# Optimization experiments

Hardware: AMD Instinct MI355X
Metric: run time of the kernel (lower is better)

## Reference

```python
import jax, jax.numpy as jnp
import numpy as np

B, N, S, CIN, COUT, GDIM = 4, 128, 8, 8, 8, 7  # batch, points, coset samples, channels, g_embed+2*q_embed


def setup_inputs() -> dict:
    key = jax.random.key(0)
    ks = jax.random.split(key, 8)
    pairwise_g = jax.random.normal(ks[0], (B, N, N, S, S, GDIM), jnp.float32)
    coset_functions = jax.random.normal(ks[1], (B, N, S, CIN), jnp.float32)
    mask = jax.random.bernoulli(ks[2], 0.9, (B, N, S))  # bool key mask (B,N,S)
    # per-channel SumKernel params: k_y = Linear(2->1), k_g = Linear(GDIM->1), stacked over CIN channels
    w_y = jax.random.normal(ks[3], (CIN, 2), jnp.float32) * 0.1
    b_y = jax.random.normal(ks[4], (CIN,), jnp.float32) * 0.1
    w_g = jax.random.normal(ks[5], (CIN, GDIM), jnp.float32) * 0.1
    b_g = jax.random.normal(ks[6], (CIN,), jnp.float32) * 0.1
    w_lin = jax.random.normal(ks[7], (COUT, CIN), jnp.float32) * (1.0 / np.sqrt(CIN))
    return {"pairwise_g": pairwise_g, "coset_functions": coset_functions, "mask": mask,
            "w_y": w_y, "b_y": b_y, "w_g": w_g, "b_g": b_g, "w_lin": w_lin}


def reference(pairwise_g, coset_functions, mask, w_y, b_y, w_g, b_g, w_lin):
    # Vectorized over the original per-channel Python loop: channel axis c.
    y = coset_functions  # (B, N, S, C)
    # k_g(pairwise_g) per channel + both biases: (B,i,j,s1,s2,C)
    logits = jnp.einsum('bijstg,cg->bijstc', pairwise_g, w_g) + (b_g + b_y)
    # k_y([y_1, y_2]): y_1 indexed by key (j, s2) -> weight w_y[:,0]; y_2 by query (i, s1) -> w_y[:,1]
    key_term = y * w_y[:, 0]   # (B, N, S, C)
    qry_term = y * w_y[:, 1]   # (B, N, S, C)
    logits = logits + key_term[:, None, :, None, :, :] + qry_term[:, :, None, :, None, :]
    # plain exp (original does NOT subtract a max), zero out masked keys (j, s2)
    att = jnp.where(mask[:, None, :, None, :, None], jnp.exp(logits), 0.0)
    att = att / att.sum(axis=(2, 4), keepdims=True)  # normalize over key dims
    # weighted sum of key values over (j, s2), residual add
    out = y + jnp.einsum('bijstc,bjtc->bisc', att, y)
    out = out * mask[..., None].astype(out.dtype)
    # output linear c_in -> c_out, no bias (torch Linear: x @ W.T)
    return out @ w_lin.T
```

## Files before the change

### kernel.cpp

```cpp
#include <hip/hip_runtime.h>


namespace {

constexpr int kN = 128, kS = 8, kC = 8, kO = 8, kG = 7;
constexpr int JSTRIDE = 68;

__global__ __launch_bounds__(512, 4)
void emha_kernel(const float* __restrict__ pg,
                 const float* __restrict__ y,
                 const int*   __restrict__ mask,
                 const float* __restrict__ w_y,
                 const float* __restrict__ w_g,
                 const float* __restrict__ w_lin,
                 float*       __restrict__ out)
{
    __shared__ float lds_kw[kN * JSTRIDE];
    __shared__ float lds_kv[kN * JSTRIDE];
    __shared__ float red[8][8][16];
    __shared__ float obuf[8][8];

    const int t  = threadIdx.x;
    const int bi = blockIdx.x;
    const int b  = bi >> 7;
    const int i  = bi & 127;

    float wg[kC][kG];
#pragma unroll
    for (int c = 0; c < kC; ++c)
#pragma unroll
        for (int g = 0; g < kG; ++g)
            wg[c][g] = w_g[c * kG + g];

    const float* yb = y    + b * (kN * kS * kC);
    const int*   mb = mask + b * (kN * kS);
    const float  wy0 = w_y[2 * (t & 7)];
#pragma unroll
    for (int k = 0; k < 16; ++k) {
        const int idx = t + k * 512;
        const float yv = yb[idx];
        const int   m  = mb[idx >> 3];
        const float kw = m ? __expf(yv * wy0) : 0.0f;
        const int off = (idx >> 6) * JSTRIDE + (idx & 63);
        lds_kw[off] = kw;
        lds_kv[off] = kw * yv;
    }
    __syncthreads();

    const int jbase = t >> 3;
    const float* pb = pg + (size_t)bi * (kN * kS * kS * kG) + (size_t)t * 56;
    float num[kC], den[kC];
#pragma unroll
    for (int c = 0; c < kC; ++c) { num[c] = 0.0f; den[c] = 0.0f; }

#pragma unroll 1
    for (int k = 0; k < 2; ++k) {
        const int j = k * 64 + jbase;
        const float* ppair = pb + k * 28672;
#pragma unroll
        for (int h = 0; h < 2; ++h) {
            float4 buf[7];
            const float4* src = reinterpret_cast<const float4*>(ppair + h * 28);
#pragma unroll
            for (int q = 0; q < 7; ++q) buf[q] = src[q];
            const float* p = reinterpret_cast<const float*>(buf);

#pragma unroll
            for (int s2i = 0; s2i < 4; ++s2i) {
                const int lo = j * JSTRIDE + (h * 4 + s2i) * 8;
                const float4 kva = *reinterpret_cast<const float4*>(&lds_kv[lo]);
                const float4 kvb = *reinterpret_cast<const float4*>(&lds_kv[lo + 4]);
                const float4 kwa = *reinterpret_cast<const float4*>(&lds_kw[lo]);
                const float4 kwb = *reinterpret_cast<const float4*>(&lds_kw[lo + 4]);
                const float kv[8] = {kva.x, kva.y, kva.z, kva.w, kvb.x, kvb.y, kvb.z, kvb.w};
                const float kw[8] = {kwa.x, kwa.y, kwa.z, kwa.w, kwb.x, kwb.y, kwb.z, kwb.w};
#pragma unroll
                for (int c = 0; c < kC; ++c) {
                    float d =      p[s2i * kG + 0] * wg[c][0];
                    d = fmaf(p[s2i * kG + 1], wg[c][1], d);
                    d = fmaf(p[s2i * kG + 2], wg[c][2], d);
                    d = fmaf(p[s2i * kG + 3], wg[c][3], d);
                    d = fmaf(p[s2i * kG + 4], wg[c][4], d);
                    d = fmaf(p[s2i * kG + 5], wg[c][5], d);
                    d = fmaf(p[s2i * kG + 6], wg[c][6], d);
                    const float e = __expf(d);
                    num[c] = fmaf(e, kv[c], num[c]);
                    den[c] = fmaf(e, kw[c], den[c]);
                }
            }
        }
    }

#pragma unroll
    for (int c = 0; c < kC; ++c) {
        num[c] += __shfl_xor(num[c], 8);
        num[c] += __shfl_xor(num[c], 16);
        num[c] += __shfl_xor(num[c], 32);
        den[c] += __shfl_xor(den[c], 8);
        den[c] += __shfl_xor(den[c], 16);
        den[c] += __shfl_xor(den[c], 32);
    }
    const int wave = t >> 6;
    const int lane = t & 63;
    if (lane < 8) {
#pragma unroll
        for (int c = 0; c < kC; ++c) {
            red[wave][lane][c]     = num[c];
            red[wave][lane][c + 8] = den[c];
        }
    }
    __syncthreads();

    if (t < 64) {
        const int s1q = t >> 3, c = t & 7;
        float ns = 0.0f, ds = 0.0f;
#pragma unroll
        for (int w = 0; w < 8; ++w) { ns += red[w][s1q][c]; ds += red[w][s1q][c + 8]; }
        const float yv = yb[(i * kS + s1q) * kC + c];
        const int   m  = mb[i * kS + s1q];
        obuf[s1q][c] = m ? (yv + ns / ds) : 0.0f;
    }
    __syncthreads();

    if (t < 64) {
        const int s1q = t >> 3, o = t & 7;
        float acc = 0.0f;
#pragma unroll
        for (int c = 0; c < kC; ++c)
            acc = fmaf(obuf[s1q][c], w_lin[o * kC + c], acc);
        out[(size_t)bi * (kS * kO) + t] = acc;
    }
}

}

extern "C" void kernel_launch(void* const* d_in, const int* in_sizes, int n_in,
                              void* d_out, int out_size, void* d_ws, size_t ws_size,
                              hipStream_t stream)
{
    const float* pg    = (const float*)d_in[0];
    const float* y     = (const float*)d_in[1];
    const int*   mask  = (const int*)  d_in[2];
    const float* w_y   = (const float*)d_in[3];
    const float* w_g   = (const float*)d_in[5];
    const float* w_lin = (const float*)d_in[7];
    float* out = (float*)d_out;

    emha_kernel<<<4 * kN, 512, 0, stream>>>(pg, y, mask, w_y, w_g, w_lin, out);
}
```

Before: 29.22 us.

## Stream pairwise_g via async global-to-LDS loads with per-wave double-stage pipeline

Each wave now owns a contiguous 16-j slab of pairwise_g. It stages that slab into LDS with global_load_lds in four chunks and prefetches the next chunk while computing the current one. The per-block key weight/value table is replaced by per-wave tiles computed just in time, which removes the initial block-wide barrier. Weights are pinned to SGPRs with readfirstlane. The cost is manual waitcnt and sched_barrier management, a fully serialized wait each iteration, and a different reduction lane mapping.

```diff
diff --git a/kernel.cpp b/kernel.cpp
--- a/kernel.cpp
+++ b/kernel.cpp
@@ -3,8 +3,15 @@
 
 namespace {
 
-constexpr int kN = 128, kS = 8, kC = 8, kO = 8, kG = 7;
-constexpr int JSTRIDE = 68;
+constexpr int kC = 8, kO = 8, kG = 7;
+
+typedef const __attribute__((address_space(1))) unsigned int* gp_t;
+typedef __attribute__((address_space(3))) unsigned int* lp_t;
+
+__device__ __forceinline__ float sgpr_pin(float x) {
+    return __int_as_float(__builtin_amdgcn_readfirstlane(__float_as_int(x)));
+}
+
 
 __global__ __launch_bounds__(512, 4)
 void emha_kernel(const float* __restrict__ pg,
@@ -15,110 +22,152 @@
                  const float* __restrict__ w_lin,
                  float*       __restrict__ out)
 {
-    __shared__ float lds_kw[kN * JSTRIDE];
-    __shared__ float lds_kv[kN * JSTRIDE];
-    __shared__ float red[8][8][16];
-    __shared__ float obuf[8][8];
+    __shared__ __align__(16) float arena[19776];
 
     const int t  = threadIdx.x;
+    const int w  = t >> 6;
+    const int l  = t & 63;
     const int bi = blockIdx.x;
     const int b  = bi >> 7;
     const int i  = bi & 127;
 
+    float* pay  = arena + w * 1792;
+    float* kwT  = arena + 14336 + w * 272;
+    float* kvT  = arena + 16512 + w * 272;
+    float* red  = arena + 18688;
+    float* obuf = arena + 19712;
+
+    const float* slab = pg + (size_t)bi * 57344;
+    const float* yb   = y    + b * 8192;
+    const int*   mb   = mask + b * 1024;
+
+    float wy0[kC];
+#pragma unroll
+    for (int c = 0; c < kC; ++c) wy0[c] = sgpr_pin(w_y[2 * c]);
     float wg[kC][kG];
 #pragma unroll
     for (int c = 0; c < kC; ++c)
 #pragma unroll
-        for (int g = 0; g < kG; ++g)
-            wg[c][g] = w_g[c * kG + g];
+        for (int g = 0; g < kG; ++g) wg[c][g] = sgpr_pin(w_g[c * kG + g]);
 
-    const float* yb = y    + b * (kN * kS * kC);
-    const int*   mb = mask + b * (kN * kS);
-    const float  wy0 = w_y[2 * (t & 7)];
+    const int w16 = l & 15;
+    const int jy  = l >> 4;
+    const int s2y = w16 >> 1;
+    const int cb  = (w16 & 1) * 4;
+    const int jl  = l >> 4;
+    const int h   = l & 1;
+
+    auto stage = [&](int g) {
+        const float* src = slab + (size_t)(w * 128 + g * 32) * 56 + l * 4;
 #pragma unroll
-    for (int k = 0; k < 16; ++k) {
-        const int idx = t + k * 512;
-        const float yv = yb[idx];
-        const int   m  = mb[idx >> 3];
-        const float kw = m ? __expf(yv * wy0) : 0.0f;
-        const int off = (idx >> 6) * JSTRIDE + (idx & 63);
-        lds_kw[off] = kw;
-        lds_kv[off] = kw * yv;
-    }
-    __syncthreads();
+        for (int q = 0; q < 7; ++q)
+            __builtin_amdgcn_global_load_lds((gp_t)(src + q * 256),
+                                             (lp_t)(pay + q * 256), 16, 0, 0);
+    };
 
-    const int jbase = t >> 3;
-    const float* pb = pg + (size_t)bi * (kN * kS * kS * kG) + (size_t)t * 56;
+    float4 yv; int mv;
+    auto loady = [&](int g) {
+        const int jg = 16 * w + 4 * g + jy;
+        yv = *reinterpret_cast<const float4*>(yb + jg * 64 + w16 * 4);
+        mv = mb[jg * 8 + s2y];
+    };
+
+    stage(0);
+    loady(0);
+
     float num[kC], den[kC];
 #pragma unroll
     for (int c = 0; c < kC; ++c) { num[c] = 0.0f; den[c] = 0.0f; }
 
 #pragma unroll 1
-    for (int k = 0; k < 2; ++k) {
-        const int j = k * 64 + jbase;
-        const float* ppair = pb + k * 28672;
+    for (int g = 0; g < 4; ++g) {
+        asm volatile("s_waitcnt vmcnt(0)" ::: "memory");
+        __builtin_amdgcn_sched_barrier(0);
+
+        {
+            const float yv4[4] = {yv.x, yv.y, yv.z, yv.w};
+            float kwq[4], kvq[4];
 #pragma unroll
-        for (int h = 0; h < 2; ++h) {
-            float4 buf[7];
-            const float4* src = reinterpret_cast<const float4*>(ppair + h * 28);
+            for (int k = 0; k < 4; ++k) {
+                const float e = __expf(yv4[k] * wy0[cb + k]);
+                kwq[k] = mv ? e : 0.0f;
+                kvq[k] = kwq[k] * yv4[k];
+            }
+            const int toff = jy * 68 + w16 * 4;
+            *reinterpret_cast<float4*>(kwT + toff) =
+                make_float4(kwq[0], kwq[1], kwq[2], kwq[3]);
+            *reinterpret_cast<float4*>(kvT + toff) =
+                make_float4(kvq[0], kvq[1], kvq[2], kvq[3]);
+        }
+
+        float4 pv[7];
+        {
+            const float4* ps = reinterpret_cast<const float4*>(pay + l * 28);
 #pragma unroll
-            for (int q = 0; q < 7; ++q) buf[q] = src[q];
-            const float* p = reinterpret_cast<const float*>(buf);
+            for (int q = 0; q < 7; ++q) pv[q] = ps[q];
+        }
+        asm volatile("s_waitcnt lgkmcnt(0)" ::: "memory");
+        __builtin_amdgcn_sched_barrier(0);
+        if (g < 3) { stage(g + 1); loady(g + 1); }
 
+        const float* pf = reinterpret_cast<const float*>(pv);
 #pragma unroll
-            for (int s2i = 0; s2i < 4; ++s2i) {
-                const int lo = j * JSTRIDE + (h * 4 + s2i) * 8;
-                const float4 kva = *reinterpret_cast<const float4*>(&lds_kv[lo]);
-                const float4 kvb = *reinterpret_cast<const float4*>(&lds_kv[lo + 4]);
-                const float4 kwa = *reinterpret_cast<const float4*>(&lds_kw[lo]);
-                const float4 kwb = *reinterpret_cast<const float4*>(&lds_kw[lo + 4]);
-                const float kv[8] = {kva.x, kva.y, kva.z, kva.w, kvb.x, kvb.y, kvb.z, kvb.w};
-                const float kw[8] = {kwa.x, kwa.y, kwa.z, kwa.w, kwb.x, kwb.y, kwb.z, kwb.w};
+        for (int s2i = 0; s2i < 4; ++s2i) {
+            const int ro = jl * 68 + (h * 4 + s2i) * 8;
+            const float4 kwa = *reinterpret_cast<const float4*>(kwT + ro);
+            const float4 kwb = *reinterpret_cast<const float4*>(kwT + ro + 4);
+            const float4 kva = *reinterpret_cast<const float4*>(kvT + ro);
+            const float4 kvb = *reinterpret_cast<const float4*>(kvT + ro + 4);
+            const float kwv[8] = {kwa.x, kwa.y, kwa.z, kwa.w,
+                                  kwb.x, kwb.y, kwb.z, kwb.w};
+            const float kvv[8] = {kva.x, kva.y, kva.z, kva.w,
+                                  kvb.x, kvb.y, kvb.z, kvb.w};
 #pragma unroll
-                for (int c = 0; c < kC; ++c) {
-                    float d =      p[s2i * kG + 0] * wg[c][0];
-                    d = fmaf(p[s2i * kG + 1], wg[c][1], d);
-                    d = fmaf(p[s2i * kG + 2], wg[c][2], d);
-                    d = fmaf(p[s2i * kG + 3], wg[c][3], d);
-                    d = fmaf(p[s2i * kG + 4], wg[c][4], d);
-                    d = fmaf(p[s2i * kG + 5], wg[c][5], d);
-                    d = fmaf(p[s2i * kG + 6], wg[c][6], d);
-                    const float e = __expf(d);
-                    num[c] = fmaf(e, kv[c], num[c]);
-                    den[c] = fmaf(e, kw[c], den[c]);
-                }
+            for (int c = 0; c < kC; ++c) {
+                float d =      pf[s2i * kG + 0] * wg[c][0];
+                d = fmaf(pf[s2i * kG + 1], wg[c][1], d);
+                d = fmaf(pf[s2i * kG + 2], wg[c][2], d);
+                d = fmaf(pf[s2i * kG + 3], wg[c][3], d);
+                d = fmaf(pf[s2i * kG + 4], wg[c][4], d);
+                d = fmaf(pf[s2i * kG + 5], wg[c][5], d);
+                d = fmaf(pf[s2i * kG + 6], wg[c][6], d);
+                const float e = __expf(d);
+                num[c] = fmaf(e, kvv[c], num[c]);
+                den[c] = fmaf(e, kwv[c], den[c]);
             }
         }
     }
 
 #pragma unroll
     for (int c = 0; c < kC; ++c) {
-        num[c] += __shfl_xor(num[c], 8);
+        num[c] += __shfl_xor(num[c], 1);
         num[c] += __shfl_xor(num[c], 16);
         num[c] += __shfl_xor(num[c], 32);
-        den[c] += __shfl_xor(den[c], 8);
+        den[c] += __shfl_xor(den[c], 1);
         den[c] += __shfl_xor(den[c], 16);
         den[c] += __shfl_xor(den[c], 32);
     }
-    const int wave = t >> 6;
-    const int lane = t & 63;
-    if (lane < 8) {
+    if (l < 16 && (l & 1) == 0) {
+        const int s1 = l >> 1;
 #pragma unroll
         for (int c = 0; c < kC; ++c) {
-            red[wave][lane][c]     = num[c];
-            red[wave][lane][c + 8] = den[c];
+            red[w * 128 + s1 * 16 + c]     = num[c];
+            red[w * 128 + s1 * 16 + 8 + c] = den[c];
         }
     }
     __syncthreads();
 
     if (t < 64) {
-        const int s1q = t >> 3, c = t & 7;
+        const int s1q = t >> 3, cc = t & 7;
         float ns = 0.0f, ds = 0.0f;
 #pragma unroll
-        for (int w = 0; w < 8; ++w) { ns += red[w][s1q][c]; ds += red[w][s1q][c + 8]; }
-        const float yv = yb[(i * kS + s1q) * kC + c];
-        const int   m  = mb[i * kS + s1q];
-        obuf[s1q][c] = m ? (yv + ns / ds) : 0.0f;
+        for (int ww = 0; ww < 8; ++ww) {
+            ns += red[ww * 128 + s1q * 16 + cc];
+            ds += red[ww * 128 + s1q * 16 + 8 + cc];
+        }
+        const float yvq = yb[(i * 8 + s1q) * 8 + cc];
+        const int   mq  = mb[i * 8 + s1q];
+        obuf[s1q * 8 + cc] = mq ? (yvq + ns / ds) : 0.0f;
     }
     __syncthreads();
 
@@ -127,8 +176,8 @@
         float acc = 0.0f;
 #pragma unroll
         for (int c = 0; c < kC; ++c)
-            acc = fmaf(obuf[s1q][c], w_lin[o * kC + c], acc);
-        out[(size_t)bi * (kS * kO) + t] = acc;
+            acc = fmaf(obuf[s1q * 8 + c], w_lin[o * kC + c], acc);
+        out[(size_t)bi * 64 + t] = acc;
     }
 }
 
@@ -146,5 +195,5 @@
     const float* w_lin = (const float*)d_in[7];
     float* out = (float*)d_out;
 
-    emha_kernel<<<4 * kN, 512, 0, stream>>>(pg, y, mask, w_y, w_g, w_lin, out);
+    emha_kernel<<<512, 512, 0, stream>>>(pg, y, mask, w_y, w_g, w_lin, out);
 }
```

New measurement: 26.92 us, median of 2. 7.9% less time.
